# Kernel optimization log

Measured on AMD Instinct MI355X. Metric: run time of the kernel, lower is better.

The kernel has to match this reference:

```python
import jax, jax.numpy as jnp
import numpy as np
from jax.ops import segment_sum

N = 50000
IN_C, HID_C, OUT_C = 128, 128, 64
ALPHA, BETA = 1.0, 0.0


def add_self_loops(edge_index, num_nodes):
    ar = jnp.arange(num_nodes, dtype=edge_index.dtype)
    loops = jnp.stack([ar, ar])  # [2, N]
    return jnp.concatenate([edge_index, loops], axis=1)


def directed_gcn_conv(x, edge_index, W, b, alpha, beta, self_loops=True):
    n = x.shape[0]
    if self_loops:
        edge_index = add_self_loops(edge_index, n)
    x = x @ W.T + b  # [N, out_c]
    row, col = edge_index[0], edge_index[1]
    ones = jnp.ones(row.shape[0], dtype=x.dtype)
    in_degree = segment_sum(ones, col, num_segments=n)
    out_degree = segment_sum(ones, row, num_segments=n)
    in_norm_inv = jnp.power(in_degree, -alpha)
    out_norm_inv = jnp.power(out_degree, -beta)
    norm = in_norm_inv[col] * out_norm_inv[row]  # [E]
    msgs = norm[:, None] * x[row]  # gather + scale: [E, out_c]
    return segment_sum(msgs, col, num_segments=n)  # scatter-add: [N, out_c]


def setup_inputs() -> dict:
    key = jax.random.key(0)
    ks = jax.random.split(key, 6)
    x = jax.random.normal(ks[0], (N, IN_C), dtype=jnp.float32)
    edge_index = jax.random.randint(ks[1], (2, 800000), 0, N, dtype=jnp.int32)
    s1 = 1.0 / np.sqrt(IN_C)
    W1 = jax.random.uniform(ks[2], (HID_C, IN_C), jnp.float32, -s1, s1)
    b1 = jax.random.uniform(ks[3], (HID_C,), jnp.float32, -s1, s1)
    s2 = 1.0 / np.sqrt(HID_C)
    W2 = jax.random.uniform(ks[4], (OUT_C, HID_C), jnp.float32, -s2, s2)
    b2 = jax.random.uniform(ks[5], (OUT_C,), jnp.float32, -s2, s2)
    return {"x": x, "edge_index": edge_index, "W1": W1, "b1": b1, "W2": W2, "b2": b2}


def reference(x, edge_index, W1, b1, W2, b2):
    h = jax.nn.relu(directed_gcn_conv(x, edge_index, W1, b1, ALPHA, BETA, True))
    out = directed_gcn_conv(h, jnp.flip(edge_index, axis=0), W2, b2, ALPHA, BETA, True)
    return out
```

## Files before the change

### kernel.cpp

```cpp
#include <hip/hip_runtime.h>

typedef unsigned int uint32;
typedef unsigned short u16;

typedef __attribute__((ext_vector_type(8))) short short8;
typedef __attribute__((ext_vector_type(4))) float f32x4;

__device__ __forceinline__ float bf16_s(u16 s) {
  uint32 v = ((uint32)s) << 16;
  return __builtin_bit_cast(float, v);
}
__device__ __forceinline__ float bf16_lo(uint32 u) {
  uint32 v = u << 16;
  return __builtin_bit_cast(float, v);
}
__device__ __forceinline__ float bf16_hi(uint32 u) {
  uint32 v = u & 0xffff0000u;
  return __builtin_bit_cast(float, v);
}
__device__ __forceinline__ u16 f2bf(float f) {
  uint32 u = __builtin_bit_cast(uint32, f);
  u += 0x7fffu + ((u >> 16) & 1u);
  return (u16)(u >> 16);
}

#define KBUK 128
#define NBUK 256
#define ABUF 48
#define BATCH 4096
#define NPBMAX 512
#define CAPB 24576
#define HS 132

__global__ __launch_bounds__(256) void detect_init(const void* __restrict__ x,
                                                   int* __restrict__ flag,
                                                   int* __restrict__ bsizes) {
  __shared__ int cnt;
  if (threadIdx.x == 0) cnt = 0;
  bsizes[threadIdx.x] = 0;
  __syncthreads();
  const u16* p = (const u16*)x;
  int c = 0;
  for (int i = threadIdx.x; i < 4096; i += 256) {
    u16 s = p[i];
    int e = (s >> 7) & 0xFF;
    c += (s == 0 || (e >= 118 && e <= 130)) ? 1 : 0;
  }
  atomicAdd(&cnt, c);
  __syncthreads();
  if (threadIdx.x == 0) *flag = (cnt > 3072) ? 1 : 0;
}

__global__ __launch_bounds__(256) void prep_count(
    const int* __restrict__ rows, const int* __restrict__ cols,
    int* __restrict__ bsizes, int E, int npb, int nCountBlk,
    const void* __restrict__ x, const void* __restrict__ W1,
    const void* __restrict__ b1, const void* __restrict__ W2,
    const void* __restrict__ b2,
    u16* __restrict__ xb, u16* __restrict__ w1b, u16* __restrict__ w2b,
    float* __restrict__ b1f, float* __restrict__ b2f,
    long nx, const int* __restrict__ flag) {
  __shared__ int h[NBUK];
  if ((int)blockIdx.x < nCountBlk) {
    int t = threadIdx.x;
    h[t] = 0;
    __syncthreads();
    int e0 = blockIdx.x * BATCH;
#pragma unroll
    for (int j = 0; j < BATCH / 256; ++j) {
      int e = e0 + j * 256 + t;
      if (e < E) {
        int r = rows[e], c = cols[e];
        atomicAdd(&h[c / npb], 1);
        atomicAdd(&h[KBUK + r / npb], 1);
      }
    }
    __syncthreads();
    if (h[t] > 0) atomicAdd(&bsizes[t], h[t]);
  } else {
    int isbf = *flag;
    long t = (long)((int)blockIdx.x - nCountBlk) * 256 + threadIdx.x;
    long o1 = nx, o2 = o1 + 128 * 128, o3 = o2 + 64 * 128, o4 = o3 + 128, o5 = o4 + 64;
    if (t < o1) {
      if (!isbf) xb[t] = f2bf(((const float*)x)[t]);
    } else if (t < o2) {
      long i = t - o1;
      w1b[i] = isbf ? ((const u16*)W1)[i] : f2bf(((const float*)W1)[i]);
    } else if (t < o3) {
      long i = t - o2;
      w2b[i] = isbf ? ((const u16*)W2)[i] : f2bf(((const float*)W2)[i]);
    } else if (t < o4) {
      long i = t - o3;
      b1f[i] = isbf ? bf16_s(((const u16*)b1)[i]) : ((const float*)b1)[i];
    } else if (t < o5) {
      long i = t - o4;
      b2f[i] = isbf ? bf16_s(((const u16*)b2)[i]) : ((const float*)b2)[i];
    }
  }
}

__global__ __launch_bounds__(256) void bucket_scan(
    const int* __restrict__ bsizes, int* __restrict__ bbase,
    int* __restrict__ gcur, int* __restrict__ offsets, int ntot) {
  __shared__ int s[NBUK];
  int t = threadIdx.x;
  int v = bsizes[t];
  s[t] = v;
  __syncthreads();
  for (int off = 1; off < 256; off <<= 1) {
    int x = (t >= off) ? s[t - off] : 0;
    __syncthreads();
    s[t] += x;
    __syncthreads();
  }
  int excl = s[t] - v;
  bbase[t] = excl;
  gcur[t] = excl;
  if (t == 255) {
    bbase[NBUK] = s[255];
    offsets[ntot] = s[255];
  }
}

__global__ __launch_bounds__(256) void gemm1_fill(
    const int* __restrict__ rows, const int* __restrict__ cols,
    int* __restrict__ gcur, uint32* __restrict__ gbuf, int E, int npb,
    int nFillBlk,
    const u16* __restrict__ Xdirect, const u16* __restrict__ Xconv,
    const u16* __restrict__ W, const float* __restrict__ Bias,
    u16* __restrict__ Y, int nrows, const int* __restrict__ flag) {
  __shared__ int lcnt[NBUK];
  __shared__ int fbase[NBUK];
  __shared__ uint32 lbuf[NBUK * ABUF];
  if ((int)blockIdx.x < nFillBlk) {
    int t = threadIdx.x;
    lcnt[t] = 0;
    __syncthreads();
    int e0 = blockIdx.x * BATCH;
#pragma unroll
    for (int j = 0; j < BATCH / 256; ++j) {
      int e = e0 + j * 256 + t;
      if (e < E) {
        int r = rows[e], c = cols[e];
        int bk1 = c / npb;
        uint32 en1 = ((uint32)(c - bk1 * npb) << 20) | (uint32)r;
        int p = atomicAdd(&lcnt[bk1], 1);
        if (p < ABUF) lbuf[bk1 * ABUF + p] = en1;
        else { int g = atomicAdd(&gcur[bk1], 1); gbuf[g] = en1; }
        int b2r = r / npb;
        int bk2 = KBUK + b2r;
        uint32 en2 = ((uint32)(r - b2r * npb) << 20) | (uint32)c;
        p = atomicAdd(&lcnt[bk2], 1);
        if (p < ABUF) lbuf[bk2 * ABUF + p] = en2;
        else { int g = atomicAdd(&gcur[bk2], 1); gbuf[g] = en2; }
      }
    }
    __syncthreads();
    int c = min(lcnt[t], ABUF);
    if (c > 0) fbase[t] = atomicAdd(&gcur[t], c);
    __syncthreads();
    int wv = t >> 6, lane = t & 63;
    for (int b = wv * 64; b < wv * 64 + 64; ++b) {
      int cb = min(lcnt[b], ABUF);
      if (cb > 0) {
        int fb = fbase[b];
        for (int jj = lane; jj < cb; jj += 64) gbuf[fb + jj] = lbuf[b * ABUF + jj];
      }
    }
  } else {
    constexpr int NT = 8;
    const u16* X = (*flag) ? Xdirect : Xconv;
    int bid = (int)blockIdx.x - nFillBlk;
    int wave = threadIdx.x >> 6;
    int lane = threadIdx.x & 63;
    int m16 = lane & 15;
    int kq = lane >> 4;
    long rowbase = (long)bid * 64 + wave * 16;
    long arow = rowbase + m16;
    if (arow >= nrows) arow = nrows - 1;
    f32x4 acc[NT];
#pragma unroll
    for (int nt = 0; nt < NT; ++nt) {
      float bv = Bias[nt * 16 + m16];
      acc[nt] = {bv, bv, bv, bv};
    }
#pragma unroll
    for (int ks = 0; ks < 4; ++ks) {
      short8 a = *(const short8*)(X + arow * 128 + ks * 32 + kq * 8);
#pragma unroll
      for (int nt = 0; nt < NT; ++nt) {
        short8 b = *(const short8*)(W + (long)(nt * 16 + m16) * 128 + ks * 32 + kq * 8);
        acc[nt] = __builtin_amdgcn_mfma_f32_16x16x32_bf16(a, b, acc[nt], 0, 0, 0);
      }
    }
    long orow0 = rowbase + kq * 4;
#pragma unroll
    for (int nt = 0; nt < NT; ++nt) {
      int col = nt * 16 + m16;
#pragma unroll
      for (int r = 0; r < 4; ++r) {
        long row = orow0 + r;
        if (row < nrows) Y[row * 128 + col] = f2bf(acc[nt][r]);
      }
    }
  }
}

__global__ __launch_bounds__(256) void csr_bucket(
    const uint32* __restrict__ gbuf, const int* __restrict__ bbase,
    int* __restrict__ offsets, int* __restrict__ idx, int N, int npb) {
  __shared__ int cnt[NPBMAX];
  __shared__ int s[NPBMAX];
  __shared__ int cur[NPBMAX];
  __shared__ int idxbuf[CAPB];
  int b = blockIdx.x;
  int t = threadIdx.x;
  int csr2 = (b >= KBUK) ? 1 : 0;
  int nb = csr2 ? b - KBUK : b;
  int base_node = nb * npb;
  int nn = N - base_node;
  if (nn > npb) nn = npb;
  if (nn < 0) nn = 0;
  int ebase = bbase[b];
  int ecnt = bbase[b + 1] - ebase;

  cnt[t] = 0; cnt[256 + t] = 0;
  cur[t] = 0; cur[256 + t] = 0;
  __syncthreads();
  for (int i = t; i < ecnt; i += 256)
    atomicAdd(&cnt[gbuf[ebase + i] >> 20], 1);
  __syncthreads();
  s[t] = cnt[t]; s[256 + t] = cnt[256 + t];
  __syncthreads();
  for (int off = 1; off < 256; off <<= 1) {
    int x0 = (t >= off) ? s[t - off] : 0;
    int x1 = (t >= off) ? s[256 + t - off] : 0;
    __syncthreads();
    s[t] += x0; s[256 + t] += x1;
    __syncthreads();
  }
  int h0 = s[255];
  __syncthreads();
  s[256 + t] += h0;
  __syncthreads();
  int obase = csr2 ? N : 0;
  for (int i = t; i < nn; i += 256)
    offsets[obase + base_node + i] = ebase + (s[i] - cnt[i]);
  bool inlds = (ecnt <= CAPB);
  __syncthreads();
  for (int i = t; i < ecnt; i += 256) {
    uint32 en = gbuf[ebase + i];
    int d = en >> 20;
    int src = (int)(en & 0xFFFFFu);
    int p = atomicAdd(&cur[d], 1);
    int pos = (s[d] - cnt[d]) + p;
    if (inlds) idxbuf[pos] = src;
    else idx[ebase + pos] = src;
  }
  __syncthreads();
  if (inlds)
    for (int i = t; i < ecnt; i += 256) idx[ebase + i] = idxbuf[i];
}

__global__ __launch_bounds__(256) void agg1_gemm2(
    const uint32* __restrict__ X, const int* __restrict__ idx,
    const int* __restrict__ offsets, const u16* __restrict__ W2,
    const float* __restrict__ Bias2, u16* __restrict__ Y2, int N, int twoE) {
  __shared__ float hl[16 * HS];
  int wv = threadIdx.x >> 6;
  int lane = threadIdx.x & 63;
  int d0 = blockIdx.x * 16;
  unsigned Nm1 = (unsigned)N - 1u;
  for (int rr = 0; rr < 4; ++rr) {
    int row = wv * 4 + rr;
    int d = d0 + row;
    int dl = min(d, N - 1);
    int beg = offsets[dl], end = offsets[dl + 1];
    if (d >= N) { beg = 0; end = 0; }
    int cntv = end - beg;
    if (beg < 0) beg = 0;
    if (end > twoE) end = twoE;
    if (end < beg) { end = beg; cntv = 0; }
    float a0 = 0.f, a1 = 0.f, b0 = 0.f, b1 = 0.f;
    float c0 = 0.f, c1 = 0.f, e0 = 0.f, e1 = 0.f;
    int i = beg;
    for (; i + 4 <= end; i += 4) {
      unsigned r0 = min((unsigned)idx[i], Nm1);
      unsigned r1 = min((unsigned)idx[i + 1], Nm1);
      unsigned r2 = min((unsigned)idx[i + 2], Nm1);
      unsigned r3 = min((unsigned)idx[i + 3], Nm1);
      uint32 u0 = X[(long)r0 * 64 + lane];
      uint32 u1 = X[(long)r1 * 64 + lane];
      uint32 u2 = X[(long)r2 * 64 + lane];
      uint32 u3 = X[(long)r3 * 64 + lane];
      a0 += bf16_lo(u0); a1 += bf16_hi(u0);
      b0 += bf16_lo(u1); b1 += bf16_hi(u1);
      c0 += bf16_lo(u2); c1 += bf16_hi(u2);
      e0 += bf16_lo(u3); e1 += bf16_hi(u3);
    }
    for (; i < end; ++i) {
      unsigned r = min((unsigned)idx[i], Nm1);
      uint32 u = X[(long)r * 64 + lane];
      a0 += bf16_lo(u); a1 += bf16_hi(u);
    }
    uint32 us = X[(long)dl * 64 + lane];
    a0 += bf16_lo(us); a1 += bf16_hi(us);
    a0 += b0 + c0 + e0;
    a1 += b1 + c1 + e1;
    float s = 1.0f / (float)(cntv + 1);
    hl[row * HS + 2 * lane]     = fmaxf(a0 * s, 0.f);
    hl[row * HS + 2 * lane + 1] = fmaxf(a1 * s, 0.f);
  }
  __syncthreads();
  int m16 = lane & 15;
  int kq = lane >> 4;
  float bv = Bias2[wv * 16 + m16];
  f32x4 acc = {bv, bv, bv, bv};
#pragma unroll
  for (int ks = 0; ks < 4; ++ks) {
    short8 a;
#pragma unroll
    for (int j = 0; j < 8; ++j)
      a[j] = (short)f2bf(hl[m16 * HS + ks * 32 + kq * 8 + j]);
    short8 b = *(const short8*)(W2 + (long)(wv * 16 + m16) * 128 + ks * 32 + kq * 8);
    acc = __builtin_amdgcn_mfma_f32_16x16x32_bf16(a, b, acc, 0, 0, 0);
  }
  int col = wv * 16 + m16;
#pragma unroll
  for (int r = 0; r < 4; ++r) {
    int row = kq * 4 + r;
    int d = d0 + row;
    if (d < N) Y2[(long)d * 64 + col] = f2bf(acc[r]);
  }
}

__global__ __launch_bounds__(256) void agg2(
    const u16* __restrict__ Y2, const int* __restrict__ idx,
    const int* __restrict__ offsets, void* __restrict__ OUT,
    const int* __restrict__ flag, int N, int twoE) {
  int w = (blockIdx.x * 256 + threadIdx.x) >> 6;
  int lane = threadIdx.x & 63;
  if (w >= N) return;
  int beg = offsets[N + w], end = offsets[N + w + 1];
  int cnt = end - beg;
  if (beg < 0) beg = 0;
  if (end > twoE) end = twoE;
  if (end < beg) end = beg;
  unsigned Nm1 = (unsigned)N - 1u;
  float a = 0.f, b = 0.f, c = 0.f, d = 0.f;
  int i = beg;
  for (; i + 4 <= end; i += 4) {
    unsigned r0 = min((unsigned)idx[i], Nm1);
    unsigned r1 = min((unsigned)idx[i + 1], Nm1);
    unsigned r2 = min((unsigned)idx[i + 2], Nm1);
    unsigned r3 = min((unsigned)idx[i + 3], Nm1);
    a += bf16_s(Y2[(long)r0 * 64 + lane]);
    b += bf16_s(Y2[(long)r1 * 64 + lane]);
    c += bf16_s(Y2[(long)r2 * 64 + lane]);
    d += bf16_s(Y2[(long)r3 * 64 + lane]);
  }
  for (; i < end; ++i) {
    unsigned r = min((unsigned)idx[i], Nm1);
    a += bf16_s(Y2[(long)r * 64 + lane]);
  }
  a += bf16_s(Y2[(long)w * 64 + lane]);
  a += b + c + d;
  float v = a / (float)(cnt + 1);
  if (*flag) ((u16*)OUT)[(long)w * 64 + lane] = f2bf(v);
  else       ((float*)OUT)[(long)w * 64 + lane] = v;
}


extern "C" void kernel_launch(void* const* d_in, const int* in_sizes, int n_in,
                              void* d_out, int out_size, void* d_ws, size_t ws_size,
                              hipStream_t stream) {
  const void* x  = d_in[0];
  const int* ei  = (const int*)d_in[1];
  const void* W1 = d_in[2];
  const void* b1 = d_in[3];
  const void* W2 = d_in[4];
  const void* b2 = d_in[5];

  int N = in_sizes[0] / 128;
  int E = in_sizes[1] / 2;
  const int* rows = ei;
  const int* cols = ei + E;

  int ntot = 2 * N;
  int npb = (N + KBUK - 1) / KBUK;
  if (npb > NPBMAX || N >= (1 << 20)) return;

  size_t o = 0;
  auto take = [&](size_t bytes) -> void* {
    void* p = (char*)d_ws + o;
    o += (bytes + 255) & ~(size_t)255;
    return p;
  };
  int* flag    = (int*)take(4);
  int* bsizes  = (int*)take(NBUK * 4);
  int* bbase   = (int*)take((NBUK + 1) * 4);
  int* gcur    = (int*)take(NBUK * 4);
  int* offsets = (int*)take((size_t)(ntot + 1) * 4);
  int* idx     = (int*)take((size_t)2 * E * 4);
  uint32* gbuf = (uint32*)take((size_t)2 * E * 4);
  u16* xb      = (u16*)take((size_t)N * 128 * 2);
  u16* w1b     = (u16*)take((size_t)128 * 128 * 2);
  u16* w2b     = (u16*)take((size_t)64 * 128 * 2);
  float* b1f   = (float*)take(128 * 4);
  float* b2f   = (float*)take(64 * 4);
  u16* y1      = (u16*)take((size_t)N * 128 * 2);
  u16* y2      = (u16*)take((size_t)N * 64 * 2);

  if (o > ws_size) return;

  long nprep = (long)N * 128 + 128 * 128 + 64 * 128 + 128 + 64;
  int nEblk = (E + BATCH - 1) / BATCH;
  int nPblk = (int)((nprep + 255) / 256);
  int nGblk = (N + 63) / 64;

  detect_init<<<1, 256, 0, stream>>>(x, flag, bsizes);
  prep_count<<<nEblk + nPblk, 256, 0, stream>>>(
      rows, cols, bsizes, E, npb, nEblk,
      x, W1, b1, W2, b2, xb, w1b, w2b, b1f, b2f, (long)N * 128, flag);
  bucket_scan<<<1, 256, 0, stream>>>(bsizes, bbase, gcur, offsets, ntot);
  gemm1_fill<<<nEblk + nGblk, 256, 0, stream>>>(
      rows, cols, gcur, gbuf, E, npb, nEblk,
      (const u16*)x, xb, w1b, b1f, y1, N, flag);
  csr_bucket<<<NBUK, 256, 0, stream>>>(gbuf, bbase, offsets, idx, N, npb);
  agg1_gemm2<<<(N + 15) / 16, 256, 0, stream>>>(
      (const uint32*)y1, idx, offsets, w2b, b2f, y2, N, 2 * E);
  agg2<<<(N + 3) / 4, 256, 0, stream>>>(y2, idx, offsets, d_out, flag, N, 2 * E);
}
```

Baseline: 220.8 us.

## Store layer-1 features as FP8 and gather two edges per wavefront

The intermediate layer-1 projection y1 is now written in FP8 (e4m3) instead of bf16, which halves the bytes gathered per edge in the first aggregation. Both aggregation kernels split each wavefront into two 32-lane halves that each handle a different edge, then combine the halves with a cross-lane shuffle, so more independent loads are in flight per wavefront. The cost is a real loss of precision in the hidden activations, which may push results past tolerance, plus an extra shuffle reduction step.

```diff
diff --git a/kernel.cpp b/kernel.cpp
--- a/kernel.cpp
+++ b/kernel.cpp
@@ -2,6 +2,7 @@
 
 typedef unsigned int uint32;
 typedef unsigned short u16;
+typedef unsigned char u8;
 
 typedef __attribute__((ext_vector_type(8))) short short8;
 typedef __attribute__((ext_vector_type(4))) float f32x4;
@@ -22,6 +23,43 @@
   uint32 u = __builtin_bit_cast(uint32, f);
   u += 0x7fffu + ((u >> 16) & 1u);
   return (u16)(u >> 16);
+}
+
+__device__ __forceinline__ void acc_fp8x4(f32x4& a, uint32 v) {
+#if __has_builtin(__builtin_amdgcn_cvt_pk_f32_fp8)
+  auto lo = __builtin_amdgcn_cvt_pk_f32_fp8((int)v, false);
+  auto hi = __builtin_amdgcn_cvt_pk_f32_fp8((int)v, true);
+  a[0] += lo[0]; a[1] += lo[1]; a[2] += hi[0]; a[3] += hi[1];
+#else
+  auto dec = [](uint32 u) -> float {
+    uint32 s = u >> 7, e = (u >> 3) & 15, m = u & 7;
+    float nrm = __builtin_bit_cast(float, (s << 31) | ((e + 120) << 23) | (m << 20));
+    float sub = (s ? -1.f : 1.f) * (float)m * (1.f / 512.f);
+    return e ? nrm : sub;
+  };
+  a[0] += dec(v & 0xFF); a[1] += dec((v >> 8) & 0xFF);
+  a[2] += dec((v >> 16) & 0xFF); a[3] += dec(v >> 24);
+#endif
+}
+__device__ __forceinline__ u8 f2fp8(float f) {
+#if __has_builtin(__builtin_amdgcn_cvt_pk_fp8_f32)
+  int p = __builtin_amdgcn_cvt_pk_fp8_f32(f, f, 0, false);
+  return (u8)(p & 0xFF);
+#else
+  uint32 b = __builtin_bit_cast(uint32, f);
+  uint32 s = (b >> 31) << 7;
+  float a = fabsf(f);
+  uint32 ab = b & 0x7fffffffu;
+  uint32 r = ab + 0x7FFFFu + ((ab >> 20) & 1u);
+  int e8 = (int)(r >> 23) - 120;
+  uint32 m = (r >> 20) & 7;
+  if (a < 0.015625f) {
+    int q = (int)(a * 512.f + 0.5f);
+    return (u8)(s | (uint32)q);
+  }
+  if (e8 > 15 || (e8 == 15 && m == 7)) return (u8)(s | 0x7E);
+  return (u8)(s | ((uint32)e8 << 3) | m);
+#endif
 }
 
 #define KBUK 128
@@ -128,7 +166,7 @@
     int nFillBlk,
     const u16* __restrict__ Xdirect, const u16* __restrict__ Xconv,
     const u16* __restrict__ W, const float* __restrict__ Bias,
-    u16* __restrict__ Y, int nrows, const int* __restrict__ flag) {
+    u8* __restrict__ Y, int nrows, const int* __restrict__ flag) {
   __shared__ int lcnt[NBUK];
   __shared__ int fbase[NBUK];
   __shared__ uint32 lbuf[NBUK * ABUF];
@@ -200,7 +238,7 @@
 #pragma unroll
       for (int r = 0; r < 4; ++r) {
         long row = orow0 + r;
-        if (row < nrows) Y[row * 128 + col] = f2bf(acc[nt][r]);
+        if (row < nrows) Y[row * 128 + col] = f2fp8(acc[nt][r]);
       }
     }
   }
@@ -263,12 +301,15 @@
 }
 
 __global__ __launch_bounds__(256) void agg1_gemm2(
-    const uint32* __restrict__ X, const int* __restrict__ idx,
+    const uint32* __restrict__ X,
+    const int* __restrict__ idx,
     const int* __restrict__ offsets, const u16* __restrict__ W2,
     const float* __restrict__ Bias2, u16* __restrict__ Y2, int N, int twoE) {
   __shared__ float hl[16 * HS];
   int wv = threadIdx.x >> 6;
   int lane = threadIdx.x & 63;
+  int half = lane >> 5;
+  int wl = lane & 31;
   int d0 = blockIdx.x * 16;
   unsigned Nm1 = (unsigned)N - 1u;
   for (int rr = 0; rr < 4; ++rr) {
@@ -281,35 +322,51 @@
     if (beg < 0) beg = 0;
     if (end > twoE) end = twoE;
     if (end < beg) { end = beg; cntv = 0; }
-    float a0 = 0.f, a1 = 0.f, b0 = 0.f, b1 = 0.f;
-    float c0 = 0.f, c1 = 0.f, e0 = 0.f, e1 = 0.f;
+    f32x4 p0 = {0, 0, 0, 0}, p1 = {0, 0, 0, 0};
+    f32x4 p2 = {0, 0, 0, 0}, p3 = {0, 0, 0, 0};
     int i = beg;
-    for (; i + 4 <= end; i += 4) {
-      unsigned r0 = min((unsigned)idx[i], Nm1);
-      unsigned r1 = min((unsigned)idx[i + 1], Nm1);
-      unsigned r2 = min((unsigned)idx[i + 2], Nm1);
-      unsigned r3 = min((unsigned)idx[i + 3], Nm1);
-      uint32 u0 = X[(long)r0 * 64 + lane];
-      uint32 u1 = X[(long)r1 * 64 + lane];
-      uint32 u2 = X[(long)r2 * 64 + lane];
-      uint32 u3 = X[(long)r3 * 64 + lane];
-      a0 += bf16_lo(u0); a1 += bf16_hi(u0);
-      b0 += bf16_lo(u1); b1 += bf16_hi(u1);
-      c0 += bf16_lo(u2); c1 += bf16_hi(u2);
-      e0 += bf16_lo(u3); e1 += bf16_hi(u3);
-    }
-    for (; i < end; ++i) {
-      unsigned r = min((unsigned)idx[i], Nm1);
-      uint32 u = X[(long)r * 64 + lane];
-      a0 += bf16_lo(u); a1 += bf16_hi(u);
-    }
-    uint32 us = X[(long)dl * 64 + lane];
-    a0 += bf16_lo(us); a1 += bf16_hi(us);
-    a0 += b0 + c0 + e0;
-    a1 += b1 + c1 + e1;
-    float s = 1.0f / (float)(cntv + 1);
-    hl[row * HS + 2 * lane]     = fmaxf(a0 * s, 0.f);
-    hl[row * HS + 2 * lane + 1] = fmaxf(a1 * s, 0.f);
+    for (; i + 16 <= end; i += 16) {
+      unsigned e0 = min((unsigned)idx[i + half], Nm1);
+      unsigned e1 = min((unsigned)idx[i + 2 + half], Nm1);
+      unsigned e2 = min((unsigned)idx[i + 4 + half], Nm1);
+      unsigned e3 = min((unsigned)idx[i + 6 + half], Nm1);
+      unsigned e4 = min((unsigned)idx[i + 8 + half], Nm1);
+      unsigned e5 = min((unsigned)idx[i + 10 + half], Nm1);
+      unsigned e6 = min((unsigned)idx[i + 12 + half], Nm1);
+      unsigned e7 = min((unsigned)idx[i + 14 + half], Nm1);
+      uint32 u0 = X[(long)e0 * 32 + wl];
+      uint32 u1 = X[(long)e1 * 32 + wl];
+      uint32 u2 = X[(long)e2 * 32 + wl];
+      uint32 u3 = X[(long)e3 * 32 + wl];
+      uint32 u4 = X[(long)e4 * 32 + wl];
+      uint32 u5 = X[(long)e5 * 32 + wl];
+      uint32 u6 = X[(long)e6 * 32 + wl];
+      uint32 u7 = X[(long)e7 * 32 + wl];
+      acc_fp8x4(p0, u0); acc_fp8x4(p1, u1);
+      acc_fp8x4(p2, u2); acc_fp8x4(p3, u3);
+      acc_fp8x4(p0, u4); acc_fp8x4(p1, u5);
+      acc_fp8x4(p2, u6); acc_fp8x4(p3, u7);
+    }
+    for (; i + 2 <= end; i += 2) {
+      unsigned e = min((unsigned)idx[i + half], Nm1);
+      acc_fp8x4(p0, X[(long)e * 32 + wl]);
+    }
+    if (half == 0) {
+      if (i < end) {
+        unsigned e = min((unsigned)idx[i], Nm1);
+        acc_fp8x4(p1, X[(long)e * 32 + wl]);
+      }
+      acc_fp8x4(p2, X[(long)dl * 32 + wl]);
+    }
+    f32x4 t4 = (p0 + p1) + (p2 + p3);
+#pragma unroll
+    for (int j = 0; j < 4; ++j) t4[j] += __shfl_xor(t4[j], 32);
+    if (half == 0) {
+      float s = 1.0f / (float)(cntv + 1);
+#pragma unroll
+      for (int j = 0; j < 4; ++j)
+        hl[row * HS + 4 * wl + j] = fmaxf(t4[j] * s, 0.f);
+    }
   }
   __syncthreads();
   int m16 = lane & 15;
@@ -329,17 +386,19 @@
 #pragma unroll
   for (int r = 0; r < 4; ++r) {
     int row = kq * 4 + r;
-    int d = d0 + row;
-    if (d < N) Y2[(long)d * 64 + col] = f2bf(acc[r]);
+    int dd = d0 + row;
+    if (dd < N) Y2[(long)dd * 64 + col] = f2bf(acc[r]);
   }
 }
 
 __global__ __launch_bounds__(256) void agg2(
-    const u16* __restrict__ Y2, const int* __restrict__ idx,
+    const uint32* __restrict__ Y2w, const int* __restrict__ idx,
     const int* __restrict__ offsets, void* __restrict__ OUT,
     const int* __restrict__ flag, int N, int twoE) {
   int w = (blockIdx.x * 256 + threadIdx.x) >> 6;
   int lane = threadIdx.x & 63;
+  int half = lane >> 5;
+  int wl = lane & 31;
   if (w >= N) return;
   int beg = offsets[N + w], end = offsets[N + w + 1];
   int cnt = end - beg;
@@ -347,27 +406,61 @@
   if (end > twoE) end = twoE;
   if (end < beg) end = beg;
   unsigned Nm1 = (unsigned)N - 1u;
-  float a = 0.f, b = 0.f, c = 0.f, d = 0.f;
+  float a0 = 0.f, a1 = 0.f, b0 = 0.f, b1 = 0.f;
+  float c0 = 0.f, c1 = 0.f, d0 = 0.f, d1 = 0.f;
   int i = beg;
-  for (; i + 4 <= end; i += 4) {
-    unsigned r0 = min((unsigned)idx[i], Nm1);
-    unsigned r1 = min((unsigned)idx[i + 1], Nm1);
-    unsigned r2 = min((unsigned)idx[i + 2], Nm1);
-    unsigned r3 = min((unsigned)idx[i + 3], Nm1);
-    a += bf16_s(Y2[(long)r0 * 64 + lane]);
-    b += bf16_s(Y2[(long)r1 * 64 + lane]);
-    c += bf16_s(Y2[(long)r2 * 64 + lane]);
-    d += bf16_s(Y2[(long)r3 * 64 + lane]);
-  }
-  for (; i < end; ++i) {
-    unsigned r = min((unsigned)idx[i], Nm1);
-    a += bf16_s(Y2[(long)r * 64 + lane]);
-  }
-  a += bf16_s(Y2[(long)w * 64 + lane]);
-  a += b + c + d;
-  float v = a / (float)(cnt + 1);
-  if (*flag) ((u16*)OUT)[(long)w * 64 + lane] = f2bf(v);
-  else       ((float*)OUT)[(long)w * 64 + lane] = v;
+  for (; i + 16 <= end; i += 16) {
+    unsigned e0 = min((unsigned)idx[i + half], Nm1);
+    unsigned e1 = min((unsigned)idx[i + 2 + half], Nm1);
+    unsigned e2 = min((unsigned)idx[i + 4 + half], Nm1);
+    unsigned e3 = min((unsigned)idx[i + 6 + half], Nm1);
+    unsigned e4 = min((unsigned)idx[i + 8 + half], Nm1);
+    unsigned e5 = min((unsigned)idx[i + 10 + half], Nm1);
+    unsigned e6 = min((unsigned)idx[i + 12 + half], Nm1);
+    unsigned e7 = min((unsigned)idx[i + 14 + half], Nm1);
+    uint32 u0 = Y2w[(long)e0 * 32 + wl];
+    uint32 u1 = Y2w[(long)e1 * 32 + wl];
+    uint32 u2 = Y2w[(long)e2 * 32 + wl];
+    uint32 u3 = Y2w[(long)e3 * 32 + wl];
+    uint32 u4 = Y2w[(long)e4 * 32 + wl];
+    uint32 u5 = Y2w[(long)e5 * 32 + wl];
+    uint32 u6 = Y2w[(long)e6 * 32 + wl];
+    uint32 u7 = Y2w[(long)e7 * 32 + wl];
+    a0 += bf16_lo(u0); a1 += bf16_hi(u0);
+    b0 += bf16_lo(u1); b1 += bf16_hi(u1);
+    c0 += bf16_lo(u2); c1 += bf16_hi(u2);
+    d0 += bf16_lo(u3); d1 += bf16_hi(u3);
+    a0 += bf16_lo(u4); a1 += bf16_hi(u4);
+    b0 += bf16_lo(u5); b1 += bf16_hi(u5);
+    c0 += bf16_lo(u6); c1 += bf16_hi(u6);
+    d0 += bf16_lo(u7); d1 += bf16_hi(u7);
+  }
+  for (; i + 2 <= end; i += 2) {
+    unsigned e = min((unsigned)idx[i + half], Nm1);
+    uint32 u = Y2w[(long)e * 32 + wl];
+    a0 += bf16_lo(u); a1 += bf16_hi(u);
+  }
+  if (half == 0) {
+    if (i < end) {
+      unsigned e = min((unsigned)idx[i], Nm1);
+      uint32 u = Y2w[(long)e * 32 + wl];
+      b0 += bf16_lo(u); b1 += bf16_hi(u);
+    }
+    uint32 u = Y2w[(long)w * 32 + wl];
+    c0 += bf16_lo(u); c1 += bf16_hi(u);
+  }
+  float t0 = (a0 + b0) + (c0 + d0);
+  float t1 = (a1 + b1) + (c1 + d1);
+  t0 += __shfl_xor(t0, 32);
+  t1 += __shfl_xor(t1, 32);
+  if (half == 0) {
+    float s = 1.0f / (float)(cnt + 1);
+    float m0 = t0 * s, m1 = t1 * s;
+    if (*flag)
+      ((uint32*)OUT)[(long)w * 32 + wl] = (uint32)f2bf(m0) | ((uint32)f2bf(m1) << 16);
+    else
+      ((float2*)OUT)[(long)w * 32 + wl] = make_float2(m0, m1);
+  }
 }
 
 
@@ -408,7 +501,7 @@
   u16* w2b     = (u16*)take((size_t)64 * 128 * 2);
   float* b1f   = (float*)take(128 * 4);
   float* b2f   = (float*)take(64 * 4);
-  u16* y1      = (u16*)take((size_t)N * 128 * 2);
+  u8* y1       = (u8*)take((size_t)N * 128);
   u16* y2      = (u16*)take((size_t)N * 64 * 2);
 
   if (o > ws_size) return;
@@ -429,5 +522,6 @@
   csr_bucket<<<NBUK, 256, 0, stream>>>(gbuf, bbase, offsets, idx, N, npb);
   agg1_gemm2<<<(N + 15) / 16, 256, 0, stream>>>(
       (const uint32*)y1, idx, offsets, w2b, b2f, y2, N, 2 * E);
-  agg2<<<(N + 3) / 4, 256, 0, stream>>>(y2, idx, offsets, d_out, flag, N, 2 * E);
-}
+  agg2<<<(N + 3) / 4, 256, 0, stream>>>(
+      (const uint32*)y2, idx, offsets, d_out, flag, N, 2 * E);
+}
```

Result: no change. 217.1 us (-1.7%).
